# Kernel tuning notes

Hardware: AMD Instinct MI355X
Metric: run time of the kernel (lower is better)

The kernel has to match this reference:

```python
import jax, jax.numpy as jnp
import numpy as np

B, S, D = 4, 1024, 768
H = 12
DK = D // H            # 64
NUM_EMB = 10
MAX_DIST = 100000.0 * 2 ** 0.5
POS_SCALE = 100000.0   # tile positions live in [0, 100000]


def setup_inputs() -> dict:
    key = jax.random.key(0)
    ks = jax.random.split(key, 12)
    query = jax.random.normal(ks[0], (B, S, D), dtype=jnp.float32)
    key_t = jax.random.normal(ks[1], (B, S, D), dtype=jnp.float32)
    value = jax.random.normal(ks[2], (B, S, D), dtype=jnp.float32)
    tile_positions = jax.random.uniform(ks[3], (B, S, 2), dtype=jnp.float32) * POS_SCALE
    # Linear weights, torch layout [out, in]; xavier_uniform init, zero bias
    lim = float(np.sqrt(6.0 / (D + D)))
    Wq = jax.random.uniform(ks[4], (D, D), minval=-lim, maxval=lim, dtype=jnp.float32)
    Wk = jax.random.uniform(ks[5], (D, D), minval=-lim, maxval=lim, dtype=jnp.float32)
    Wv = jax.random.uniform(ks[6], (D, D), minval=-lim, maxval=lim, dtype=jnp.float32)
    bq = jnp.zeros((D,), jnp.float32)
    bk = jnp.zeros((D,), jnp.float32)
    bv = jnp.zeros((D,), jnp.float32)
    emb_k = jax.random.normal(ks[7], (NUM_EMB, DK), dtype=jnp.float32)  # nn.Embedding default N(0,1)
    return {"query": query, "key": key_t, "value": value,
            "tile_positions": tile_positions,
            "Wq": Wq, "bq": bq, "Wk": Wk, "bk": bk, "Wv": Wv, "bv": bv,
            "emb_k": emb_k}


def reference(query, key, value, tile_positions, Wq, bq, Wk, bk, Wv, bv, emb_k):
    b, s, _ = query.shape
    # projections -> [B, H, S, DK]
    q = (query @ Wq.T + bq).reshape(b, s, H, DK).transpose(0, 2, 1, 3)
    k = (key   @ Wk.T + bk).reshape(b, s, H, DK).transpose(0, 2, 1, 3)
    v = (value @ Wv.T + bv).reshape(b, s, H, DK).transpose(0, 2, 1, 3)
    # pairwise distances, normalized, discretized to embedding indices
    pos = jax.lax.stop_gradient(tile_positions)
    diff = pos[:, :, None, :] - pos[:, None, :, :]          # [B,S,S,2]
    dist = jnp.sqrt(jnp.sum(diff * diff, axis=-1)) / MAX_DIST  # [B,S,S]
    idx = jnp.clip(jnp.round(dist * (NUM_EMB - 1)), 0, NUM_EMB - 1).astype(jnp.int32)
    rk = emb_k[idx]                                          # [B,S,S,DK]
    # logits: QK^T plus distance-aware key bias
    attn_logits = jnp.einsum('bhqd,bhkd->bhqk', q, k)
    attn_logits = attn_logits + jnp.einsum('bhqd,bqkd->bhqk', q, rk)
    attn_logits = attn_logits / (DK ** 0.5)
    attention = jax.nn.softmax(attn_logits, axis=-1)
    out = jnp.einsum('bhqk,bhkd->bhqd', attention, v)       # [B,H,S,DK]
    out = out.transpose(0, 2, 1, 3).reshape(b, s, -1)       # [B,S,D]
    return out
```

## Files before the change

### kernel.cpp

```cpp
#include <hip/hip_runtime.h>
#include <hip/hip_bf16.h>

#define Bsz 4
#define Ssz 1024
#define Dsz 768
#define Hn 12
#define DKsz 64
#define NUMEMB 10

#define POSF_OFF 64
#define EMBF_OFF 32832
#define IDX_OFF  35392
#define K_OFF    4229696
#define V_OFF    10521152

#define BM 64
#define BN 128
#define BK 32
#define LPAD 40

#define IPAD 80

typedef __attribute__((ext_vector_type(8))) short short8;
typedef __attribute__((ext_vector_type(8))) float float8;
typedef __attribute__((ext_vector_type(4))) float f32x4;
typedef __attribute__((ext_vector_type(4))) unsigned int u32x4;

__device__ __forceinline__ float bfbits2f(short u) {
    union { unsigned int i; float f; } v;
    v.i = ((unsigned int)(unsigned short)u) << 16;
    return v.f;
}
__device__ __forceinline__ unsigned short f2bf_bits(float f) {
    __hip_bfloat16 h = __float2bfloat16(f);
    return *reinterpret_cast<unsigned short*>(&h);
}

template<bool BF16>
__device__ __forceinline__ float loadf(const void* base, size_t idx) {
    if constexpr (BF16) return __bfloat162float(((const __hip_bfloat16*)base)[idx]);
    else return ((const float*)base)[idx];
}
template<bool BF16>
__device__ __forceinline__ short8 load8bf(const void* base, size_t idx) {
    if constexpr (BF16) {
        return *(const short8*)((const short*)base + idx);
    } else {
        float8 f = *(const float8*)((const float*)base + idx);
        short8 r;
#pragma unroll
        for (int i = 0; i < 8; i++) r[i] = (short)f2bf_bits(f[i]);
        return r;
    }
}

__global__ __launch_bounds__(64) void detect_kernel(
    const unsigned int* __restrict__ q, const unsigned int* __restrict__ p,
    const unsigned int* __restrict__ w, const unsigned int* __restrict__ e,
    int* __restrict__ flags)
{
    const int which = blockIdx.x;
    const unsigned int* ptr = (which == 0) ? q : ((which == 1) ? p : ((which == 2) ? w : e));
    const int n = (which == 3) ? 320 : ((which == 1) ? 4096 : 1024);
    int cnt = 0;
    for (int i = threadIdx.x; i < n; i += 64) {
        const unsigned int ex = (ptr[i] >> 7) & 0xFF;
        cnt += (ex >= 110 && ex <= 145) ? 1 : 0;
    }
#pragma unroll
    for (int off = 1; off < 64; off <<= 1) cnt += __shfl_xor(cnt, off, 64);
    if (threadIdx.x == 0) flags[which] = (2 * cnt > n) ? 1 : 0;
}

__global__ __launch_bounds__(256) void prep_kernel(
    const void* __restrict__ pos, const void* __restrict__ emb,
    const int* __restrict__ flags, float* __restrict__ posf, float* __restrict__ embf)
{
    const bool pb = flags[1] != 0, eb = flags[3] != 0;
    const int t0 = blockIdx.x * 256 + threadIdx.x;
    for (int i = t0; i < Bsz * Ssz * 2; i += 1024)
        posf[i] = pb ? loadf<true>(pos, i) : loadf<false>(pos, i);
    for (int i = t0; i < NUMEMB * DKsz; i += 1024)
        embf[i] = eb ? loadf<true>(emb, i) : loadf<false>(emb, i);
}

__global__ __launch_bounds__(256) void idx_kernel(
    const float* __restrict__ posf, unsigned char* __restrict__ idxb)
{
    const int kt = blockIdx.x, qt = blockIdx.y, b = blockIdx.z;
    const int t = threadIdx.x;
    const int r = t >> 2, cc = t & 3;
    const int q = qt * 64 + r;
    const float qx = posf[((size_t)b * Ssz + q) * 2];
    const float qy = posf[((size_t)b * Ssz + q) * 2 + 1];
    const float MAXD = 141421.35623730951f;
    const int k0 = kt * 64 + cc * 16;
    unsigned int w[4];
#pragma unroll
    for (int g = 0; g < 4; g++) {
        unsigned int acc = 0;
#pragma unroll
        for (int u = 0; u < 4; u++) {
            const int k = k0 + g * 4 + u;
            const float kx = posf[((size_t)b * Ssz + k) * 2];
            const float ky = posf[((size_t)b * Ssz + k) * 2 + 1];
            const float dx = __fsub_rn(qx, kx);
            const float dy = __fsub_rn(qy, ky);
            const float ss = __fadd_rn(__fmul_rn(dx, dx), __fmul_rn(dy, dy));
            const float dist = __fdiv_rn(sqrtf(ss), MAXD);
            const float d9 = __fmul_rn(dist, 9.0f);
            int idx = (int)rintf(d9);
            idx = idx < 0 ? 0 : (idx > NUMEMB - 1 ? NUMEMB - 1 : idx);
            acc |= ((unsigned int)idx) << (8 * u);
        }
        w[g] = acc;
    }
    u32x4 v; v[0] = w[0]; v[1] = w[1]; v[2] = w[2]; v[3] = w[3];
    *(u32x4*)(idxb + ((size_t)(b * Ssz + q)) * Ssz + k0) = v;
}

template<bool XB, bool WB>
__device__ __forceinline__ void proj_body(
    const void* X, const void* W, const void* bias, void* Y, bool ybf,
    int bx, int by, short* As, short* Bs)
{
    const int tid  = threadIdx.x;
    const int wave = tid >> 6;
    const int lane = tid & 63;
    const int l15  = lane & 15;
    const int quad = lane >> 4;
    const int wm = wave & 1;
    const int wn = wave >> 1;
    const int m0 = bx * BM;
    const int n0 = by * BN;

    f32x4 acc[2][4];
#pragma unroll
    for (int i = 0; i < 2; i++)
#pragma unroll
        for (int j = 0; j < 4; j++) acc[i][j] = (f32x4)0.0f;

    const int r0 = tid >> 2;
    const int cc = tid & 3;

    short8 pa  = load8bf<XB>(X, (size_t)(m0 + r0)      * Dsz + cc * 8);
    short8 pb0 = load8bf<WB>(W, (size_t)(n0 + r0)      * Dsz + cc * 8);
    short8 pb1 = load8bf<WB>(W, (size_t)(n0 + 64 + r0) * Dsz + cc * 8);

    for (int kk = 0; kk < Dsz; kk += BK) {
        __syncthreads();
        *(short8*)&As[(r0)      * LPAD + cc * 8] = pa;
        *(short8*)&Bs[(r0)      * LPAD + cc * 8] = pb0;
        *(short8*)&Bs[(64 + r0) * LPAD + cc * 8] = pb1;
        __syncthreads();

        if (kk + BK < Dsz) {
            pa  = load8bf<XB>(X, (size_t)(m0 + r0)      * Dsz + kk + BK + cc * 8);
            pb0 = load8bf<WB>(W, (size_t)(n0 + r0)      * Dsz + kk + BK + cc * 8);
            pb1 = load8bf<WB>(W, (size_t)(n0 + 64 + r0) * Dsz + kk + BK + cc * 8);
        }

        short8 af[2], bf[4];
#pragma unroll
        for (int i = 0; i < 2; i++)
            af[i] = *(const short8*)&As[(wm * 32 + i * 16 + l15) * LPAD + quad * 8];
#pragma unroll
        for (int j = 0; j < 4; j++)
            bf[j] = *(const short8*)&Bs[(wn * 64 + j * 16 + l15) * LPAD + quad * 8];
#pragma unroll
        for (int i = 0; i < 2; i++)
#pragma unroll
            for (int j = 0; j < 4; j++)
                acc[i][j] = __builtin_amdgcn_mfma_f32_16x16x32_bf16(af[i], bf[j], acc[i][j], 0, 0, 0);
    }

#pragma unroll
    for (int j = 0; j < 4; j++) {
        const int n = n0 + wn * 64 + j * 16 + l15;
        const float bv_ = loadf<WB>(bias, n);
#pragma unroll
        for (int i = 0; i < 2; i++) {
#pragma unroll
            for (int r = 0; r < 4; r++) {
                const int m = m0 + wm * 32 + i * 16 + quad * 4 + r;
                const float val = acc[i][j][r] + bv_;
                if (ybf) ((__hip_bfloat16*)Y)[(size_t)m * Dsz + n] = __float2bfloat16(val);
                else     ((float*)Y)[(size_t)m * Dsz + n] = val;
            }
        }
    }
}

__global__ __launch_bounds__(256) void proj_kernel(
    const void* X0, const void* X1, const void* X2,
    const void* Wq, const void* bq, const void* Wk, const void* bk,
    const void* Wv, const void* bv,
    void* Qw, void* Kw, void* Vw, const int* __restrict__ flags)
{
    __shared__ __align__(16) short As[BM * LPAD];
    __shared__ __align__(16) short Bs[BN * LPAD];
    const int z = blockIdx.z;
    const void* X = (z == 0) ? X0 : ((z == 1) ? X1 : X2);
    const void* W = (z == 0) ? Wq : ((z == 1) ? Wk : Wv);
    const void* B = (z == 0) ? bq : ((z == 1) ? bk : bv);
    void* Y = (z == 0) ? Qw : ((z == 1) ? Kw : Vw);
    const bool xb = flags[0] != 0, wb = flags[2] != 0;
    const bool ybf = xb || (z != 0);
    if (xb) { if (wb) proj_body<true , true >(X, W, B, Y, ybf, blockIdx.x, blockIdx.y, As, Bs);
              else    proj_body<true , false>(X, W, B, Y, ybf, blockIdx.x, blockIdx.y, As, Bs); }
    else    { if (wb) proj_body<false, true >(X, W, B, Y, ybf, blockIdx.x, blockIdx.y, As, Bs);
              else    proj_body<false, false>(X, W, B, Y, ybf, blockIdx.x, blockIdx.y, As, Bs); }
}

template<bool QB>
__device__ __forceinline__ void attn_body(
    const void* Qw, const short* __restrict__ Ks, const short* __restrict__ Vs,
    const unsigned char* __restrict__ idxb, const float* __restrict__ embf, void* out,
    unsigned short* Klds, unsigned short* Vtlds, unsigned short* Plds,
    float* qe, unsigned char* Ilds)
{
    const int qt = blockIdx.x, h = blockIdx.y, b = blockIdx.z;
    const int tid  = threadIdx.x;
    const int wave = tid >> 6;
    const int lane = tid & 63;
    const int l15  = lane & 15;
    const int quad = lane >> 4;

    for (int p = tid; p < 64 * NUMEMB; p += 256) {
        const int row = p / NUMEMB, e = p - row * NUMEMB;
        const size_t qoff = ((size_t)b * Ssz + qt * 64 + row) * Dsz + h * DKsz;
        float s = 0.f;
#pragma unroll
        for (int c = 0; c < 8; c++) {
            short8 qv = load8bf<QB>(Qw, qoff + c * 8);
            const float* er = embf + e * DKsz + c * 8;
#pragma unroll
            for (int i = 0; i < 8; i++) s += bfbits2f(qv[i]) * er[i];
        }
        qe[p] = s;
    }

    short8 qfrag[2];
    {
        const size_t qbase = ((size_t)b * Ssz + qt * 64 + wave * 16 + l15) * Dsz + h * DKsz;
        qfrag[0] = load8bf<QB>(Qw, qbase + quad * 8);
        qfrag[1] = load8bf<QB>(Qw, qbase + 32 + quad * 8);
    }

    float m_run[4], l_run[4];
    f32x4 oacc[4];
#pragma unroll
    for (int r = 0; r < 4; r++) { m_run[r] = -1e30f; l_run[r] = 0.f; }
#pragma unroll
    for (int j = 0; j < 4; j++) oacc[j] = (f32x4)0.0f;

    const int srow = tid >> 3, schk = tid & 7;
    const int irow = tid >> 2, ichk = tid & 3;

    short8 pk0, pk1, pv0, pv1;
    u32x4 pidx;
    {
        pk0 = *(const short8*)(Ks + ((size_t)b * Ssz + srow)      * Dsz + h * DKsz + schk * 8);
        pk1 = *(const short8*)(Ks + ((size_t)b * Ssz + 32 + srow) * Dsz + h * DKsz + schk * 8);
        pv0 = *(const short8*)(Vs + ((size_t)b * Ssz + srow)      * Dsz + h * DKsz + schk * 8);
        pv1 = *(const short8*)(Vs + ((size_t)b * Ssz + 32 + srow) * Dsz + h * DKsz + schk * 8);
        pidx = *(const u32x4*)(idxb + ((size_t)(b * Ssz + qt * 64 + irow)) * Ssz + ichk * 16);
    }

    for (int it = 0; it < 16; it++) {
        __syncthreads();
        *(short8*)&Klds[(srow)      * 72 + schk * 8] = pk0;
        *(short8*)&Klds[(32 + srow) * 72 + schk * 8] = pk1;
        {
            const int ssw0 = srow        ^ (schk << 3);
            const int ssw1 = (32 + srow) ^ (schk << 3);
#pragma unroll
            for (int i = 0; i < 8; i++) {
                Vtlds[(schk * 8 + i) * 72 + ssw0] = (unsigned short)pv0[i];
                Vtlds[(schk * 8 + i) * 72 + ssw1] = (unsigned short)pv1[i];
            }
        }
        *(u32x4*)&Ilds[irow * IPAD + ichk * 16] = pidx;
        __syncthreads();

        if (it + 1 < 16) {
            const size_t kb = ((size_t)b * Ssz + (it + 1) * 64) * Dsz + h * DKsz;
            pk0 = *(const short8*)(Ks + kb + (size_t)srow * Dsz + schk * 8);
            pk1 = *(const short8*)(Ks + kb + (size_t)(32 + srow) * Dsz + schk * 8);
            pv0 = *(const short8*)(Vs + kb + (size_t)srow * Dsz + schk * 8);
            pv1 = *(const short8*)(Vs + kb + (size_t)(32 + srow) * Dsz + schk * 8);
            pidx = *(const u32x4*)(idxb + ((size_t)(b * Ssz + qt * 64 + irow)) * Ssz + (it + 1) * 64 + ichk * 16);
        }

        f32x4 sf[4];
#pragma unroll
        for (int j = 0; j < 4; j++) sf[j] = (f32x4)0.0f;
#pragma unroll
        for (int st = 0; st < 2; st++) {
#pragma unroll
            for (int j = 0; j < 4; j++) {
                short8 kb2 = *(const short8*)&Klds[(j * 16 + l15) * 72 + st * 32 + quad * 8];
                sf[j] = __builtin_amdgcn_mfma_f32_16x16x32_bf16(qfrag[st], kb2, sf[j], 0, 0, 0);
            }
        }

        float sv[4][4];
#pragma unroll
        for (int r = 0; r < 4; r++) {
            const int m = wave * 16 + quad * 4 + r;
#pragma unroll
            for (int j = 0; j < 4; j++) {
                const int n = j * 16 + l15;
                const int idx = Ilds[m * IPAD + n];
                sv[r][j] = (sf[j][r] + qe[m * NUMEMB + idx]) * 0.125f;
            }
        }

        float alpha[4];
#pragma unroll
        for (int r = 0; r < 4; r++) {
            float vmax = sv[r][0];
#pragma unroll
            for (int j = 1; j < 4; j++) vmax = fmaxf(vmax, sv[r][j]);
#pragma unroll
            for (int off = 1; off < 16; off <<= 1) vmax = fmaxf(vmax, __shfl_xor(vmax, off, 16));
            const float mnew = fmaxf(m_run[r], vmax);
            alpha[r] = __expf(m_run[r] - mnew);
            m_run[r] = mnew;
            float psum = 0.f;
#pragma unroll
            for (int j = 0; j < 4; j++) {
                const float p = __expf(sv[r][j] - mnew);
                sv[r][j] = p;
                psum += p;
            }
#pragma unroll
            for (int off = 1; off < 16; off <<= 1) psum += __shfl_xor(psum, off, 16);
            l_run[r] = l_run[r] * alpha[r] + psum;
        }
#pragma unroll
        for (int j = 0; j < 4; j++) {
            f32x4 o = oacc[j];
#pragma unroll
            for (int r = 0; r < 4; r++) o[r] *= alpha[r];
            oacc[j] = o;
        }

#pragma unroll
        for (int r = 0; r < 4; r++) {
            const int m = wave * 16 + quad * 4 + r;
#pragma unroll
            for (int j = 0; j < 4; j++) {
                const int csw = (j * 16 + l15) ^ (quad << 4);
                Plds[m * 72 + csw] = f2bf_bits(sv[r][j]);
            }
        }

#pragma unroll
        for (int st = 0; st < 2; st++) {
            const int prow = wave * 16 + l15;
            const int pcsw = (st * 32 + quad * 8) ^ ((l15 >> 2) << 4);
            short8 pf = *(const short8*)&Plds[prow * 72 + pcsw];
#pragma unroll
            for (int j = 0; j < 4; j++) {
                const int d = j * 16 + l15;
                const int vsw = (st * 32 + quad * 8) ^ (((d >> 3) & 7) << 3);
                short8 vb = *(const short8*)&Vtlds[d * 72 + vsw];
                oacc[j] = __builtin_amdgcn_mfma_f32_16x16x32_bf16(pf, vb, oacc[j], 0, 0, 0);
            }
        }
    }

    __syncthreads();

#pragma unroll
    for (int r = 0; r < 4; r++) {
        const float inv = 1.0f / l_run[r];
        const int m = qt * 64 + wave * 16 + quad * 4 + r;
#pragma unroll
        for (int j = 0; j < 4; j++) {
            const int n = h * DKsz + j * 16 + l15;
            const float val = oacc[j][r] * inv;
            const size_t oidx = ((size_t)b * Ssz + m) * Dsz + n;
            if constexpr (QB) ((__hip_bfloat16*)out)[oidx] = __float2bfloat16(val);
            else              ((float*)out)[oidx] = val;
        }
    }
}

__global__ __launch_bounds__(256) void attn_kernel(
    const void* Qw, const short* __restrict__ Ks, const short* __restrict__ Vs,
    const unsigned char* __restrict__ idxb, const float* __restrict__ embf, void* out,
    const int* __restrict__ flags)
{
    __shared__ __align__(16) unsigned short Klds[64 * 72];
    __shared__ __align__(16) unsigned short Vtlds[64 * 72];
    __shared__ __align__(16) unsigned short Plds[64 * 72];
    __shared__ __align__(16) float qe[64 * NUMEMB];
    __shared__ __align__(16) unsigned char Ilds[64 * IPAD];

    if (flags[0] != 0)
        attn_body<true >(Qw, Ks, Vs, idxb, embf, out, Klds, Vtlds, Plds, qe, Ilds);
    else
        attn_body<false>(Qw, Ks, Vs, idxb, embf, out, Klds, Vtlds, Plds, qe, Ilds);
}

extern "C" void kernel_launch(void* const* d_in, const int* in_sizes, int n_in,
                              void* d_out, int out_size, void* d_ws, size_t ws_size,
                              hipStream_t stream) {
    const void* query = d_in[0];
    const void* key   = d_in[1];
    const void* value = d_in[2];
    const void* tpos  = d_in[3];
    const void* Wq    = d_in[4];
    const void* bq    = d_in[5];
    const void* Wk    = d_in[6];
    const void* bk    = d_in[7];
    const void* Wv    = d_in[8];
    const void* bv    = d_in[9];
    const void* emb   = d_in[10];

    int*           flags = (int*)d_ws;
    float*         posf  = (float*)((char*)d_ws + POSF_OFF);
    float*         embf  = (float*)((char*)d_ws + EMBF_OFF);
    unsigned char* idxb  = (unsigned char*)d_ws + IDX_OFF;
    void*          Kw    = (char*)d_ws + K_OFF;
    void*          Vw    = (char*)d_ws + V_OFF;
    void*          Qw    = d_out;

    detect_kernel<<<4, 64, 0, stream>>>(
        (const unsigned int*)query, (const unsigned int*)tpos,
        (const unsigned int*)Wq, (const unsigned int*)emb, flags);

    prep_kernel<<<4, 256, 0, stream>>>(tpos, emb, flags, posf, embf);

    idx_kernel<<<dim3(16, 16, Bsz), 256, 0, stream>>>(posf, idxb);

    proj_kernel<<<dim3(64, 6, 3), 256, 0, stream>>>(
        query, key, value, Wq, bq, Wk, bk, Wv, bv, Qw, Kw, Vw, flags);

    attn_kernel<<<dim3(16, Hn, Bsz), 256, 0, stream>>>(
        Qw, (const short*)Kw, (const short*)Vw, idxb, embf, d_out, flags);
}
```

Before: 241.3 us.

## Use DPP row reductions, packed V-transpose LDS writes, transposed idx tile reads

Replaces the shfl_xor-based 16-lane max/sum reductions in the online softmax with DPP row operations (quad_perm and row_ror), which avoids the LDS-permute path. V rows are now loaded as adjacent pairs so the transposed LDS store writes packed 32-bit words instead of 16-bit scalars. The distance-index tile is loaded transposed (relying on idx symmetry), so each lane fetches four row indices with one 32-bit LDS read. The transposed index read assumes the index matrix is symmetric, which holds for pairwise distances, and the DPP row_ror pattern must reproduce the full 16-lane reduction.

```diff
diff --git a/kernel.cpp b/kernel.cpp
--- a/kernel.cpp
+++ b/kernel.cpp
@@ -34,6 +34,27 @@
 __device__ __forceinline__ unsigned short f2bf_bits(float f) {
     __hip_bfloat16 h = __float2bfloat16(f);
     return *reinterpret_cast<unsigned short*>(&h);
+}
+
+template<int CTRL>
+__device__ __forceinline__ float dppf(float x) {
+    int xi = __float_as_int(x);
+    int r = __builtin_amdgcn_update_dpp(xi, xi, CTRL, 0xF, 0xF, true);
+    return __int_as_float(r);
+}
+__device__ __forceinline__ float red_max16(float v) {
+    v = fmaxf(v, dppf<0xB1>(v));
+    v = fmaxf(v, dppf<0x4E>(v));
+    v = fmaxf(v, dppf<0x124>(v));
+    v = fmaxf(v, dppf<0x128>(v));
+    return v;
+}
+__device__ __forceinline__ float red_sum16(float v) {
+    v += dppf<0xB1>(v);
+    v += dppf<0x4E>(v);
+    v += dppf<0x124>(v);
+    v += dppf<0x128>(v);
+    return v;
 }
 
 template<bool BF16>
@@ -255,16 +276,17 @@
     for (int j = 0; j < 4; j++) oacc[j] = (f32x4)0.0f;
 
     const int srow = tid >> 3, schk = tid & 7;
+    const int vp   = tid >> 3;
     const int irow = tid >> 2, ichk = tid & 3;
 
     short8 pk0, pk1, pv0, pv1;
     u32x4 pidx;
     {
-        pk0 = *(const short8*)(Ks + ((size_t)b * Ssz + srow)      * Dsz + h * DKsz + schk * 8);
-        pk1 = *(const short8*)(Ks + ((size_t)b * Ssz + 32 + srow) * Dsz + h * DKsz + schk * 8);
-        pv0 = *(const short8*)(Vs + ((size_t)b * Ssz + srow)      * Dsz + h * DKsz + schk * 8);
-        pv1 = *(const short8*)(Vs + ((size_t)b * Ssz + 32 + srow) * Dsz + h * DKsz + schk * 8);
-        pidx = *(const u32x4*)(idxb + ((size_t)(b * Ssz + qt * 64 + irow)) * Ssz + ichk * 16);
+        pk0 = *(const short8*)(Ks + ((size_t)b * Ssz + srow)       * Dsz + h * DKsz + schk * 8);
+        pk1 = *(const short8*)(Ks + ((size_t)b * Ssz + 32 + srow)  * Dsz + h * DKsz + schk * 8);
+        pv0 = *(const short8*)(Vs + ((size_t)b * Ssz + 2 * vp)     * Dsz + h * DKsz + schk * 8);
+        pv1 = *(const short8*)(Vs + ((size_t)b * Ssz + 2 * vp + 1) * Dsz + h * DKsz + schk * 8);
+        pidx = *(const u32x4*)(idxb + ((size_t)(b * Ssz + irow)) * Ssz + qt * 64 + ichk * 16);
     }
 
     for (int it = 0; it < 16; it++) {
@@ -272,12 +294,12 @@
         *(short8*)&Klds[(srow)      * 72 + schk * 8] = pk0;
         *(short8*)&Klds[(32 + srow) * 72 + schk * 8] = pk1;
         {
-            const int ssw0 = srow        ^ (schk << 3);
-            const int ssw1 = (32 + srow) ^ (schk << 3);
+            const int ssw = (2 * vp) ^ (schk << 3);
 #pragma unroll
             for (int i = 0; i < 8; i++) {
-                Vtlds[(schk * 8 + i) * 72 + ssw0] = (unsigned short)pv0[i];
-                Vtlds[(schk * 8 + i) * 72 + ssw1] = (unsigned short)pv1[i];
+                const unsigned int dw = (unsigned int)(unsigned short)pv0[i]
+                                      | ((unsigned int)(unsigned short)pv1[i] << 16);
+                *(unsigned int*)&Vtlds[(schk * 8 + i) * 72 + ssw] = dw;
             }
         }
         *(u32x4*)&Ilds[irow * IPAD + ichk * 16] = pidx;
@@ -287,9 +309,9 @@
             const size_t kb = ((size_t)b * Ssz + (it + 1) * 64) * Dsz + h * DKsz;
             pk0 = *(const short8*)(Ks + kb + (size_t)srow * Dsz + schk * 8);
             pk1 = *(const short8*)(Ks + kb + (size_t)(32 + srow) * Dsz + schk * 8);
-            pv0 = *(const short8*)(Vs + kb + (size_t)srow * Dsz + schk * 8);
-            pv1 = *(const short8*)(Vs + kb + (size_t)(32 + srow) * Dsz + schk * 8);
-            pidx = *(const u32x4*)(idxb + ((size_t)(b * Ssz + qt * 64 + irow)) * Ssz + (it + 1) * 64 + ichk * 16);
+            pv0 = *(const short8*)(Vs + kb + (size_t)(2 * vp) * Dsz + schk * 8);
+            pv1 = *(const short8*)(Vs + kb + (size_t)(2 * vp + 1) * Dsz + schk * 8);
+            pidx = *(const u32x4*)(idxb + ((size_t)(b * Ssz + (it + 1) * 64 + irow)) * Ssz + qt * 64 + ichk * 16);
         }
 
         f32x4 sf[4];
@@ -306,24 +328,21 @@
 
         float sv[4][4];
 #pragma unroll
+        for (int j = 0; j < 4; j++) {
+            const unsigned int iw = *(const unsigned int*)&Ilds[(j * 16 + l15) * IPAD + wave * 16 + quad * 4];
+#pragma unroll
+            for (int r = 0; r < 4; r++) {
+                const int m = wave * 16 + quad * 4 + r;
+                const int idx = (iw >> (8 * r)) & 0xFF;
+                sv[r][j] = (sf[j][r] + qe[m * NUMEMB + idx]) * 0.125f;
+            }
+        }
+
+        float alpha[4];
+#pragma unroll
         for (int r = 0; r < 4; r++) {
-            const int m = wave * 16 + quad * 4 + r;
-#pragma unroll
-            for (int j = 0; j < 4; j++) {
-                const int n = j * 16 + l15;
-                const int idx = Ilds[m * IPAD + n];
-                sv[r][j] = (sf[j][r] + qe[m * NUMEMB + idx]) * 0.125f;
-            }
-        }
-
-        float alpha[4];
-#pragma unroll
-        for (int r = 0; r < 4; r++) {
-            float vmax = sv[r][0];
-#pragma unroll
-            for (int j = 1; j < 4; j++) vmax = fmaxf(vmax, sv[r][j]);
-#pragma unroll
-            for (int off = 1; off < 16; off <<= 1) vmax = fmaxf(vmax, __shfl_xor(vmax, off, 16));
+            float vmax = fmaxf(fmaxf(sv[r][0], sv[r][1]), fmaxf(sv[r][2], sv[r][3]));
+            vmax = red_max16(vmax);
             const float mnew = fmaxf(m_run[r], vmax);
             alpha[r] = __expf(m_run[r] - mnew);
             m_run[r] = mnew;
@@ -334,8 +353,7 @@
                 sv[r][j] = p;
                 psum += p;
             }
-#pragma unroll
-            for (int off = 1; off < 16; off <<= 1) psum += __shfl_xor(psum, off, 16);
+            psum = red_sum16(psum);
             l_run[r] = l_run[r] * alpha[r] + psum;
         }
 #pragma unroll
```

Result: faster. 229.7 us (-4.8%).
